# Optimization experiments

Measured on AMD Instinct MI355X. Metric: run time of the kernel, lower is better.

Reference implementation:

```python
import jax, jax.numpy as jnp
import numpy as np

B, NQ, NK, D = 4, 4096, 4096, 256


def setup_inputs() -> dict:
    key = jax.random.key(0)
    ks = jax.random.split(key, 14)
    s = 1.0 / np.sqrt(D)
    def lin(k):
        kw, kb = jax.random.split(k)
        return (jax.random.uniform(kw, (D, D), jnp.float32, -s, s),
                jax.random.uniform(kb, (D,), jnp.float32, -s, s))
    Wq, bq = lin(ks[0]); Wk, bk = lin(ks[1]); Wv, bv = lin(ks[2])
    W1, b1 = lin(ks[3]); W2, b2 = lin(ks[4]); W3, b3 = lin(ks[5])
    x = jax.random.normal(ks[6], (B, NK, D), jnp.float32)
    query = jax.random.normal(ks[7], (B, NQ, D), jnp.float32)
    return {"x": x, "query": query,
            "Wq": Wq, "bq": bq, "Wk": Wk, "bk": bk, "Wv": Wv, "bv": bv,
            "W1": W1, "b1": b1, "W2": W2, "b2": b2, "W3": W3, "b3": b3}


def reference(x, query, Wq, bq, Wk, bk, Wv, bv, W1, b1, W2, b2, W3, b3):
    # Linear: y = x @ W.T + b (torch convention)
    q = jnp.einsum('bnd,ed->bne', query, Wq) + bq   # [B,NQ,D]
    k = jnp.einsum('bnd,ed->bne', x, Wk) + bk       # [B,NK,D]
    v = jnp.einsum('bnd,ed->bne', x, Wv) + bv       # [B,NK,D]
    scale = 1.0 / jnp.sqrt(jnp.float32(x.shape[-1]))
    scores = jnp.einsum('bqd,bkd->bqk', q, k) * scale  # [B,NQ,NK]
    attn = jax.nn.softmax(scores, axis=-1)
    out = jnp.einsum('bqk,bkd->bqd', attn, v)          # [B,NQ,D]
    h = jax.nn.relu(jnp.einsum('bqd,ed->bqe', out, W1) + b1)
    h = jax.nn.relu(jnp.einsum('bqd,ed->bqe', h, W2) + b2)
    h = jax.nn.relu(jnp.einsum('bqd,ed->bqe', h, W3) + b3)
    return h, attn
```

## Files before the change

kernel.cpp:

```cpp
#include <hip/hip_runtime.h>

typedef _Float16 h16;
typedef __attribute__((ext_vector_type(4))) _Float16 h16x4;
typedef __attribute__((ext_vector_type(8))) _Float16 h16x8;
typedef __attribute__((ext_vector_type(4))) float f32x4;

#define NQD 4194304L
#define NROWS 16384L
#define NKK 4096L

static __device__ __forceinline__ f32x4 mfma16(h16x8 a, h16x8 b, f32x4 c) {
  return __builtin_amdgcn_mfma_f32_16x16x32_f16(a, b, c, 0, 0, 0);
}

__global__ void cast_weights(const float* __restrict__ w0, const float* __restrict__ w1,
                             const float* __restrict__ w2, const float* __restrict__ w3,
                             const float* __restrict__ w4, const float* __restrict__ w5,
                             h16* __restrict__ dst) {
  int wi = blockIdx.y;
  const float* src = wi == 0 ? w0 : wi == 1 ? w1 : wi == 2 ? w2 : wi == 3 ? w3 : wi == 4 ? w4 : w5;
  int c = blockIdx.x * 256 + threadIdx.x;
  float4 v = ((const float4*)src)[c];
  h16x4 h = {(h16)v.x, (h16)v.y, (h16)v.z, (h16)v.w};
  *(h16x4*)&dst[(long)wi * 65536 + (long)c * 4] = h;
}

__global__ __launch_bounds__(256) void qkv_proj(const float* __restrict__ x,
                                                const float* __restrict__ qry,
                                                const h16* __restrict__ wh,
                                                const float* __restrict__ bq,
                                                const float* __restrict__ bk,
                                                const float* __restrict__ bv,
                                                h16* __restrict__ qh,
                                                h16* __restrict__ kh,
                                                h16* __restrict__ vT) {
  const int z = blockIdx.z;
  const float* A = (z == 0) ? qry : x;
  const h16* W = wh + (long)z * 65536;
  const float* bias = (z == 0) ? bq : (z == 1) ? bk : bv;
  h16* outH = (z == 0) ? qh : (z == 1) ? kh : nullptr;
  h16* outT = (z == 2) ? vT : nullptr;

  __shared__ h16 As[128][72];
  __shared__ h16 Bs[64][72];
  const int tid = threadIdx.x;
  const int wave = tid >> 6, lane = tid & 63;
  const int quad = lane >> 4, l16 = lane & 15;
  const long arow0 = (long)blockIdx.x * 128;
  const int bn = blockIdx.y;
  f32x4 acc[2][4] = {};
  for (int k0 = 0; k0 < 256; k0 += 64) {
    #pragma unroll
    for (int it = 0; it < 8; ++it) {
      int c = it * 256 + tid;
      int r = c >> 4, c4 = (c & 15) * 4;
      float4 v = *(const float4*)&A[(arow0 + r) * 256 + k0 + c4];
      h16x4 h = {(h16)v.x, (h16)v.y, (h16)v.z, (h16)v.w};
      *(h16x4*)&As[r][c4] = h;
    }
    #pragma unroll
    for (int it = 0; it < 2; ++it) {
      int c = it * 256 + tid;
      int r = c >> 3, c8 = (c & 7) * 8;
      *(h16x8*)&Bs[r][c8] = *(const h16x8*)&W[(long)(bn * 64 + r) * 256 + k0 + c8];
    }
    __syncthreads();
    #pragma unroll
    for (int ks = 0; ks < 64; ks += 32) {
      h16x8 a[2], b[4];
      #pragma unroll
      for (int mi = 0; mi < 2; ++mi)
        a[mi] = *(const h16x8*)&As[wave * 32 + mi * 16 + l16][ks + quad * 8];
      #pragma unroll
      for (int ni = 0; ni < 4; ++ni)
        b[ni] = *(const h16x8*)&Bs[ni * 16 + l16][ks + quad * 8];
      #pragma unroll
      for (int mi = 0; mi < 2; ++mi)
        #pragma unroll
        for (int ni = 0; ni < 4; ++ni)
          acc[mi][ni] = mfma16(a[mi], b[ni], acc[mi][ni]);
    }
    __syncthreads();
  }
  #pragma unroll
  for (int mi = 0; mi < 2; ++mi) {
    #pragma unroll
    for (int ni = 0; ni < 4; ++ni) {
      int n = bn * 64 + ni * 16 + l16;
      float bv_ = bias[n];
      #pragma unroll
      for (int i = 0; i < 4; ++i) {
        long m = arow0 + wave * 32 + mi * 16 + quad * 4 + i;
        float v = acc[mi][ni][i] + bv_;
        if (outH) outH[m * 256 + n] = (h16)v;
        if (outT) outT[((m >> 12) * 256 + n) * 4096L + (m & 4095)] = (h16)v;
      }
    }
  }
}

__global__ __launch_bounds__(256) void gemm256(const h16* __restrict__ A,
                                               const h16* __restrict__ W,
                                               const float* __restrict__ bias,
                                               h16* __restrict__ outH,
                                               float* __restrict__ outF) {
  __shared__ h16 As[128][72];
  __shared__ h16 Bs[64][72];
  const int tid = threadIdx.x;
  const int wave = tid >> 6, lane = tid & 63;
  const int quad = lane >> 4, l16 = lane & 15;
  const long arow0 = (long)blockIdx.x * 128;
  const int bn = blockIdx.y;
  f32x4 acc[2][4] = {};
  for (int k0 = 0; k0 < 256; k0 += 64) {
    #pragma unroll
    for (int it = 0; it < 4; ++it) {
      int c = it * 256 + tid;
      int r = c >> 3, c8 = (c & 7) * 8;
      *(h16x8*)&As[r][c8] = *(const h16x8*)&A[(arow0 + r) * 256 + k0 + c8];
    }
    #pragma unroll
    for (int it = 0; it < 2; ++it) {
      int c = it * 256 + tid;
      int r = c >> 3, c8 = (c & 7) * 8;
      *(h16x8*)&Bs[r][c8] = *(const h16x8*)&W[(long)(bn * 64 + r) * 256 + k0 + c8];
    }
    __syncthreads();
    #pragma unroll
    for (int ks = 0; ks < 64; ks += 32) {
      h16x8 a[2], b[4];
      #pragma unroll
      for (int mi = 0; mi < 2; ++mi)
        a[mi] = *(const h16x8*)&As[wave * 32 + mi * 16 + l16][ks + quad * 8];
      #pragma unroll
      for (int ni = 0; ni < 4; ++ni)
        b[ni] = *(const h16x8*)&Bs[ni * 16 + l16][ks + quad * 8];
      #pragma unroll
      for (int mi = 0; mi < 2; ++mi)
        #pragma unroll
        for (int ni = 0; ni < 4; ++ni)
          acc[mi][ni] = mfma16(a[mi], b[ni], acc[mi][ni]);
    }
    __syncthreads();
  }
  #pragma unroll
  for (int mi = 0; mi < 2; ++mi) {
    #pragma unroll
    for (int ni = 0; ni < 4; ++ni) {
      int n = bn * 64 + ni * 16 + l16;
      float bv = bias[n];
      #pragma unroll
      for (int i = 0; i < 4; ++i) {
        long m = arow0 + wave * 32 + mi * 16 + quad * 4 + i;
        float v = fmaxf(acc[mi][ni][i] + bv, 0.0f);
        if (outH) outH[m * 256 + n] = (h16)v;
        if (outF) outF[m * 256 + n] = v;
      }
    }
  }
}

__global__ __launch_bounds__(256) void gemm_scores(const h16* __restrict__ qh,
                                                   const h16* __restrict__ kh,
                                                   float2* __restrict__ stats,
                                                   h16* __restrict__ Sh,
                                                   float* __restrict__ Sf) {
  __shared__ h16 As[128][72];
  __shared__ h16 Bs[128][72];
  const int tid = threadIdx.x;
  const int wave = tid >> 6, lane = tid & 63;
  const int quad = lane >> 4, l16 = lane & 15;
  const int bm = blockIdx.x, bn = blockIdx.y, b = blockIdx.z;
  const h16* Aq = qh + (long)b * 4096 * 256 + (long)bm * 128 * 256;
  const h16* Bk = kh + (long)b * 4096 * 256 + (long)bn * 128 * 256;
  f32x4 acc[2][8] = {};
  for (int k0 = 0; k0 < 256; k0 += 64) {
    #pragma unroll
    for (int it = 0; it < 4; ++it) {
      int c = it * 256 + tid;
      int r = c >> 3, c8 = (c & 7) * 8;
      *(h16x8*)&As[r][c8] = *(const h16x8*)&Aq[(long)r * 256 + k0 + c8];
      *(h16x8*)&Bs[r][c8] = *(const h16x8*)&Bk[(long)r * 256 + k0 + c8];
    }
    __syncthreads();
    #pragma unroll
    for (int ks = 0; ks < 64; ks += 32) {
      h16x8 a[2], bb[8];
      #pragma unroll
      for (int mi = 0; mi < 2; ++mi)
        a[mi] = *(const h16x8*)&As[wave * 32 + mi * 16 + l16][ks + quad * 8];
      #pragma unroll
      for (int ni = 0; ni < 8; ++ni)
        bb[ni] = *(const h16x8*)&Bs[ni * 16 + l16][ks + quad * 8];
      #pragma unroll
      for (int mi = 0; mi < 2; ++mi)
        #pragma unroll
        for (int ni = 0; ni < 8; ++ni)
          acc[mi][ni] = mfma16(a[mi], bb[ni], acc[mi][ni]);
    }
    __syncthreads();
  }
  #pragma unroll
  for (int mi = 0; mi < 2; ++mi)
    #pragma unroll
    for (int ni = 0; ni < 8; ++ni)
      #pragma unroll
      for (int i = 0; i < 4; ++i)
        acc[mi][ni][i] *= 0.0625f;
  #pragma unroll
  for (int mi = 0; mi < 2; ++mi) {
    #pragma unroll
    for (int i = 0; i < 4; ++i) {
      float mx = -1e30f;
      #pragma unroll
      for (int ni = 0; ni < 8; ++ni) mx = fmaxf(mx, acc[mi][ni][i]);
      #pragma unroll
      for (int off = 1; off < 16; off <<= 1) mx = fmaxf(mx, __shfl_xor(mx, off));
      float es = 0.0f;
      #pragma unroll
      for (int ni = 0; ni < 8; ++ni) es += __expf(acc[mi][ni][i] - mx);
      #pragma unroll
      for (int off = 1; off < 16; off <<= 1) es += __shfl_xor(es, off);
      if (l16 == 0) {
        long row = (long)b * 4096 + bm * 128 + wave * 32 + mi * 16 + quad * 4 + i;
        stats[row * 32 + bn] = make_float2(mx, es);
      }
    }
  }
  #pragma unroll
  for (int mi = 0; mi < 2; ++mi) {
    #pragma unroll
    for (int ni = 0; ni < 8; ++ni) {
      long col = (long)bn * 128 + ni * 16 + l16;
      #pragma unroll
      for (int i = 0; i < 4; ++i) {
        long row = (long)b * 4096 + bm * 128 + wave * 32 + mi * 16 + quad * 4 + i;
        if (Sh) Sh[row * 4096 + col] = (h16)acc[mi][ni][i];
        else    Sf[row * 4096 + col] = acc[mi][ni][i];
      }
    }
  }
}

__global__ __launch_bounds__(256) void rowstats_reduce(const float2* __restrict__ stats,
                                                       float2* __restrict__ rowstats) {
  const int tid = threadIdx.x;
  const int wave = tid >> 6, lane = tid & 63;
  const int j = lane & 31, rr = lane >> 5;
  const long base = (long)blockIdx.x * 256 + wave * 64;
  for (int it = 0; it < 32; ++it) {
    long row = base + it * 2 + rr;
    float2 s = stats[row * 32 + j];
    float m = s.x;
    #pragma unroll
    for (int off = 1; off < 32; off <<= 1) m = fmaxf(m, __shfl_xor(m, off));
    float e = s.y * __expf(s.x - m);
    #pragma unroll
    for (int off = 1; off < 32; off <<= 1) e += __shfl_xor(e, off);
    if (j == 0) rowstats[row] = make_float2(m, 1.0f / e);
  }
}

template <typename TS>
__global__ __launch_bounds__(256, 4) void gemm_av(const TS* __restrict__ S,
                                                  const h16* __restrict__ vT,
                                                  const float2* __restrict__ rowstats,
                                                  float* __restrict__ attn,
                                                  float* __restrict__ Opart,
                                                  h16* __restrict__ Odirect,
                                                  int KS) {
  __shared__ h16 As[64][40];
  __shared__ h16 Bs[256][40];
  const int tid = threadIdx.x;
  const int wave = tid >> 6, lane = tid & 63;
  const int quad = lane >> 4, l16 = lane & 15;
  const int mb = blockIdx.x, kc = blockIdx.y;
  const int KB = 4096 / KS;
  const long row0 = (long)mb * 64;
  const int b = mb >> 6;
  const h16* Vb = vT + (long)b * 256 * 4096;

  const int sr = tid >> 2, sc = (tid & 3) * 8;
  const long srow = row0 + sr;
  const float2 st = rowstats[srow];
  const TS* Srow = S + srow * 4096;
  float* Arow = attn + srow * 4096;

  f32x4 acc[4][4] = {};
  const int kbeg = kc * KB, kend = kbeg + KB;
  for (int k0 = kbeg; k0 < kend; k0 += 32) {
    float p[8];
    if constexpr (sizeof(TS) == 2) {
      h16x8 sv = *(const h16x8*)&Srow[k0 + sc];
      #pragma unroll
      for (int e = 0; e < 8; ++e) p[e] = __expf((float)sv[e] - st.x) * st.y;
    } else {
      float4 sa = *(const float4*)&Srow[k0 + sc];
      float4 sb = *(const float4*)&Srow[k0 + sc + 4];
      p[0] = __expf(sa.x - st.x) * st.y; p[1] = __expf(sa.y - st.x) * st.y;
      p[2] = __expf(sa.z - st.x) * st.y; p[3] = __expf(sa.w - st.x) * st.y;
      p[4] = __expf(sb.x - st.x) * st.y; p[5] = __expf(sb.y - st.x) * st.y;
      p[6] = __expf(sb.z - st.x) * st.y; p[7] = __expf(sb.w - st.x) * st.y;
    }
    float4 w0 = {p[0], p[1], p[2], p[3]}, w1 = {p[4], p[5], p[6], p[7]};
    *(float4*)&Arow[k0 + sc] = w0;
    *(float4*)&Arow[k0 + sc + 4] = w1;
    h16x8 ph = {(h16)p[0], (h16)p[1], (h16)p[2], (h16)p[3],
                (h16)p[4], (h16)p[5], (h16)p[6], (h16)p[7]};
    *(h16x8*)&As[sr][sc] = ph;
    #pragma unroll
    for (int it = 0; it < 4; ++it) {
      int d = it * 64 + (tid >> 2);
      *(h16x8*)&Bs[d][sc] = *(const h16x8*)&Vb[(long)d * 4096 + k0 + sc];
    }
    __syncthreads();
    h16x8 a[4], bb[4];
    #pragma unroll
    for (int mi = 0; mi < 4; ++mi)
      a[mi] = *(const h16x8*)&As[mi * 16 + l16][quad * 8];
    #pragma unroll
    for (int ni = 0; ni < 4; ++ni)
      bb[ni] = *(const h16x8*)&Bs[wave * 64 + ni * 16 + l16][quad * 8];
    #pragma unroll
    for (int mi = 0; mi < 4; ++mi)
      #pragma unroll
      for (int ni = 0; ni < 4; ++ni)
        acc[mi][ni] = mfma16(a[mi], bb[ni], acc[mi][ni]);
    __syncthreads();
  }
  #pragma unroll
  for (int mi = 0; mi < 4; ++mi) {
    #pragma unroll
    for (int ni = 0; ni < 4; ++ni) {
      int col = wave * 64 + ni * 16 + l16;
      #pragma unroll
      for (int i = 0; i < 4; ++i) {
        long row = row0 + mi * 16 + quad * 4 + i;
        if (Opart) Opart[((long)kc * NROWS + row) * 256 + col] = acc[mi][ni][i];
        else       Odirect[row * 256 + col] = (h16)acc[mi][ni][i];
      }
    }
  }
}

__global__ __launch_bounds__(256) void reduce_O(const float* __restrict__ Opart,
                                                h16* __restrict__ oh) {
  long i4 = (long)blockIdx.x * 256 + threadIdx.x;
  float4 s = {0, 0, 0, 0};
  #pragma unroll
  for (int kc = 0; kc < 4; ++kc) {
    float4 t = *(const float4*)&Opart[kc * NQD + i4 * 4];
    s.x += t.x; s.y += t.y; s.z += t.z; s.w += t.w;
  }
  h16x4 h = {(h16)s.x, (h16)s.y, (h16)s.z, (h16)s.w};
  *(h16x4*)&oh[i4 * 4] = h;
}

extern "C" void kernel_launch(void* const* d_in, const int* in_sizes, int n_in,
                              void* d_out, int out_size, void* d_ws, size_t ws_size,
                              hipStream_t stream) {
  (void)in_sizes; (void)n_in; (void)out_size;
  const float* x   = (const float*)d_in[0];
  const float* qry = (const float*)d_in[1];
  const float* Wq  = (const float*)d_in[2];  const float* bq = (const float*)d_in[3];
  const float* Wk  = (const float*)d_in[4];  const float* bk = (const float*)d_in[5];
  const float* Wv  = (const float*)d_in[6];  const float* bv = (const float*)d_in[7];
  const float* W1  = (const float*)d_in[8];  const float* b1 = (const float*)d_in[9];
  const float* W2  = (const float*)d_in[10]; const float* b2 = (const float*)d_in[11];
  const float* W3  = (const float*)d_in[12]; const float* b3 = (const float*)d_in[13];

  float* outH = (float*)d_out;
  float* attn = outH + NQD;

  char* w = (char*)d_ws;
  h16* qh = (h16*)w;
  h16* kh = qh + NQD;
  h16* vT = kh + NQD;
  h16* oh = vT + NQD;
  h16* h1 = oh + NQD;
  h16* h2 = h1 + NQD;
  h16* wh = h2 + NQD;
  size_t off_rs   = (size_t)(6 * NQD + 6 * 65536) * 2;
  size_t BASE     = off_rs + NROWS * 8;
  size_t statsB   = NROWS * 32 * 8;
  size_t ShB      = NROWS * NKK * 2;
  size_t OpartB   = 4 * NQD * 4;

  bool modeA = ws_size >= BASE + statsB + ShB + OpartB;
  bool modeB = !modeA && ws_size >= BASE + statsB + OpartB;

  float2* stats    = (modeA || modeB) ? (float2*)(w + BASE) : (float2*)oh;
  float2* rowstats = (modeA || modeB) ? (float2*)(w + off_rs) : (float2*)h2;
  h16*    Sh       = modeA ? (h16*)(w + BASE + statsB) : nullptr;
  float*  Opart    = modeA ? (float*)(w + BASE + statsB + ShB)
                   : modeB ? (float*)(w + BASE + statsB) : nullptr;
  int KS = (modeA || modeB) ? 4 : 1;

  cast_weights<<<dim3(64, 6), 256, 0, stream>>>(Wq, Wk, Wv, W1, W2, W3, wh);
  qkv_proj<<<dim3(128, 4, 3), 256, 0, stream>>>(x, qry, wh, bq, bk, bv, qh, kh, vT);
  gemm_scores<<<dim3(32, 32, 4), 256, 0, stream>>>(qh, kh, stats, Sh, modeA ? nullptr : attn);
  rowstats_reduce<<<dim3(64), 256, 0, stream>>>(stats, rowstats);
  if (modeA)
    gemm_av<h16><<<dim3(256, KS), 256, 0, stream>>>(Sh, vT, rowstats, attn, Opart, oh, KS);
  else
    gemm_av<float><<<dim3(256, KS), 256, 0, stream>>>(attn, vT, rowstats, attn, Opart, oh, KS);
  if (Opart)
    reduce_O<<<dim3(4096), 256, 0, stream>>>(Opart, oh);
  gemm256<<<dim3(128, 4), 256, 0, stream>>>(oh, wh + 3 * 65536, b1, h1, nullptr);
  gemm256<<<dim3(128, 4), 256, 0, stream>>>(h1, wh + 4 * 65536, b2, h2, nullptr);
  gemm256<<<dim3(128, 4), 256, 0, stream>>>(h2, wh + 5 * 65536, b3, nullptr, outH);
}
```

Baseline: 660.1 us.

## Fuse rowstats reduce into gemm_av, stage transposed/score stores through LDS, nontemporal attn writes

```diff
diff --git a/kernel.cpp b/kernel.cpp
--- a/kernel.cpp
+++ b/kernel.cpp
@@ -41,8 +41,9 @@
   h16* outH = (z == 0) ? qh : (z == 1) ? kh : nullptr;
   h16* outT = (z == 2) ? vT : nullptr;
 
-  __shared__ h16 As[128][72];
-  __shared__ h16 Bs[64][72];
+  __shared__ h16 smem[128 * 72 + 64 * 72];
+  h16 (*As)[72] = (h16(*)[72])smem;
+  h16 (*Bs)[72] = (h16(*)[72])(smem + 128 * 72);
   const int tid = threadIdx.x;
   const int wave = tid >> 6, lane = tid & 63;
   const int quad = lane >> 4, l16 = lane & 15;
@@ -82,19 +83,43 @@
     }
     __syncthreads();
   }
-  #pragma unroll
-  for (int mi = 0; mi < 2; ++mi) {
-    #pragma unroll
-    for (int ni = 0; ni < 4; ++ni) {
-      int n = bn * 64 + ni * 16 + l16;
-      float bv_ = bias[n];
-      #pragma unroll
-      for (int i = 0; i < 4; ++i) {
-        long m = arow0 + wave * 32 + mi * 16 + quad * 4 + i;
-        float v = acc[mi][ni][i] + bv_;
-        if (outH) outH[m * 256 + n] = (h16)v;
-        if (outT) outT[((m >> 12) * 256 + n) * 4096L + (m & 4095)] = (h16)v;
-      }
+  if (outH) {
+    #pragma unroll
+    for (int mi = 0; mi < 2; ++mi) {
+      #pragma unroll
+      for (int ni = 0; ni < 4; ++ni) {
+        int n = bn * 64 + ni * 16 + l16;
+        float bv_ = bias[n];
+        #pragma unroll
+        for (int i = 0; i < 4; ++i) {
+          long m = arow0 + wave * 32 + mi * 16 + quad * 4 + i;
+          outH[m * 256 + n] = (h16)(acc[mi][ni][i] + bv_);
+        }
+      }
+    }
+  } else {
+    h16* stg = smem;
+    #pragma unroll
+    for (int mi = 0; mi < 2; ++mi) {
+      #pragma unroll
+      for (int ni = 0; ni < 4; ++ni) {
+        int dl = ni * 16 + l16;
+        float bv_ = bias[bn * 64 + dl];
+        int mlb = wave * 32 + mi * 16 + quad * 4;
+        h16x4 hv = {(h16)(acc[mi][ni][0] + bv_), (h16)(acc[mi][ni][1] + bv_),
+                    (h16)(acc[mi][ni][2] + bv_), (h16)(acc[mi][ni][3] + bv_)};
+        *(h16x4*)&stg[dl * 136 + mlb] = hv;
+      }
+    }
+    __syncthreads();
+    const int bb = (int)(arow0 >> 12);
+    const long kb = arow0 & 4095;
+    #pragma unroll
+    for (int p = 0; p < 4; ++p) {
+      int d = p * 16 + (tid >> 4);
+      int c = (tid & 15) * 8;
+      h16x8 v = *(const h16x8*)&stg[d * 136 + c];
+      *(h16x8*)&outT[((long)bb * 256 + bn * 64 + d) * 4096 + kb + c] = v;
     }
   }
 }
@@ -165,8 +190,9 @@
                                                    float2* __restrict__ stats,
                                                    h16* __restrict__ Sh,
                                                    float* __restrict__ Sf) {
-  __shared__ h16 As[128][72];
-  __shared__ h16 Bs[128][72];
+  __shared__ h16 smem[128 * 72 * 2];
+  h16 (*As)[72] = (h16(*)[72])smem;
+  h16 (*Bs)[72] = (h16(*)[72])(smem + 128 * 72);
   const int tid = threadIdx.x;
   const int wave = tid >> 6, lane = tid & 63;
   const int quad = lane >> 4, l16 = lane & 15;
@@ -227,50 +253,57 @@
       }
     }
   }
-  #pragma unroll
-  for (int mi = 0; mi < 2; ++mi) {
-    #pragma unroll
-    for (int ni = 0; ni < 8; ++ni) {
-      long col = (long)bn * 128 + ni * 16 + l16;
-      #pragma unroll
-      for (int i = 0; i < 4; ++i) {
-        long row = (long)b * 4096 + bm * 128 + wave * 32 + mi * 16 + quad * 4 + i;
-        if (Sh) Sh[row * 4096 + col] = (h16)acc[mi][ni][i];
-        else    Sf[row * 4096 + col] = acc[mi][ni][i];
-      }
-    }
-  }
-}
-
-__global__ __launch_bounds__(256) void rowstats_reduce(const float2* __restrict__ stats,
-                                                       float2* __restrict__ rowstats) {
-  const int tid = threadIdx.x;
-  const int wave = tid >> 6, lane = tid & 63;
-  const int j = lane & 31, rr = lane >> 5;
-  const long base = (long)blockIdx.x * 256 + wave * 64;
-  for (int it = 0; it < 32; ++it) {
-    long row = base + it * 2 + rr;
-    float2 s = stats[row * 32 + j];
-    float m = s.x;
-    #pragma unroll
-    for (int off = 1; off < 32; off <<= 1) m = fmaxf(m, __shfl_xor(m, off));
-    float e = s.y * __expf(s.x - m);
-    #pragma unroll
-    for (int off = 1; off < 32; off <<= 1) e += __shfl_xor(e, off);
-    if (j == 0) rowstats[row] = make_float2(m, 1.0f / e);
+  if (Sh) {
+    h16* stg = smem;
+    #pragma unroll
+    for (int mi = 0; mi < 2; ++mi) {
+      #pragma unroll
+      for (int ni = 0; ni < 8; ++ni) {
+        int c = ni * 16 + l16;
+        #pragma unroll
+        for (int i = 0; i < 4; ++i) {
+          int r = wave * 32 + mi * 16 + quad * 4 + i;
+          stg[r * 136 + c] = (h16)acc[mi][ni][i];
+        }
+      }
+    }
+    __syncthreads();
+    const long rowbase = (long)b * 4096 + (long)bm * 128;
+    const long colbase = (long)bn * 128;
+    #pragma unroll
+    for (int p = 0; p < 8; ++p) {
+      int r = p * 16 + (tid >> 4);
+      int c = (tid & 15) * 8;
+      h16x8 v = *(const h16x8*)&stg[r * 136 + c];
+      *(h16x8*)&Sh[(rowbase + r) * 4096 + colbase + c] = v;
+    }
+  } else {
+    #pragma unroll
+    for (int mi = 0; mi < 2; ++mi) {
+      #pragma unroll
+      for (int ni = 0; ni < 8; ++ni) {
+        long col = (long)bn * 128 + ni * 16 + l16;
+        #pragma unroll
+        for (int i = 0; i < 4; ++i) {
+          long row = (long)b * 4096 + bm * 128 + wave * 32 + mi * 16 + quad * 4 + i;
+          Sf[row * 4096 + col] = acc[mi][ni][i];
+        }
+      }
+    }
   }
 }
 
 template <typename TS>
 __global__ __launch_bounds__(256, 4) void gemm_av(const TS* __restrict__ S,
                                                   const h16* __restrict__ vT,
-                                                  const float2* __restrict__ rowstats,
+                                                  const float2* __restrict__ stats,
                                                   float* __restrict__ attn,
                                                   float* __restrict__ Opart,
                                                   h16* __restrict__ Odirect,
                                                   int KS) {
   __shared__ h16 As[64][40];
   __shared__ h16 Bs[256][40];
+  __shared__ float2 rs[64];
   const int tid = threadIdx.x;
   const int wave = tid >> 6, lane = tid & 63;
   const int quad = lane >> 4, l16 = lane & 15;
@@ -280,9 +313,27 @@
   const int b = mb >> 6;
   const h16* Vb = vT + (long)b * 256 * 4096;
 
+  {
+    int r = tid >> 2, j = tid & 3;
+    const float2* sp = stats + (row0 + r) * 32 + j * 8;
+    float2 sv[8];
+    float m = -1e30f;
+    #pragma unroll
+    for (int t = 0; t < 8; ++t) { sv[t] = sp[t]; m = fmaxf(m, sv[t].x); }
+    m = fmaxf(m, __shfl_xor(m, 1));
+    m = fmaxf(m, __shfl_xor(m, 2));
+    float e = 0.0f;
+    #pragma unroll
+    for (int t = 0; t < 8; ++t) e += sv[t].y * __expf(sv[t].x - m);
+    e += __shfl_xor(e, 1);
+    e += __shfl_xor(e, 2);
+    if (j == 0) rs[r] = make_float2(m, 1.0f / e);
+  }
+  __syncthreads();
+
   const int sr = tid >> 2, sc = (tid & 3) * 8;
   const long srow = row0 + sr;
-  const float2 st = rowstats[srow];
+  const float2 st = rs[sr];
   const TS* Srow = S + srow * 4096;
   float* Arow = attn + srow * 4096;
 
@@ -302,9 +353,9 @@
       p[4] = __expf(sb.x - st.x) * st.y; p[5] = __expf(sb.y - st.x) * st.y;
       p[6] = __expf(sb.z - st.x) * st.y; p[7] = __expf(sb.w - st.x) * st.y;
     }
-    float4 w0 = {p[0], p[1], p[2], p[3]}, w1 = {p[4], p[5], p[6], p[7]};
-    *(float4*)&Arow[k0 + sc] = w0;
-    *(float4*)&Arow[k0 + sc + 4] = w1;
+    f32x4 w0 = {p[0], p[1], p[2], p[3]}, w1 = {p[4], p[5], p[6], p[7]};
+    __builtin_nontemporal_store(w0, (f32x4*)&Arow[k0 + sc]);
+    __builtin_nontemporal_store(w1, (f32x4*)&Arow[k0 + sc + 4]);
     h16x8 ph = {(h16)p[0], (h16)p[1], (h16)p[2], (h16)p[3],
                 (h16)p[4], (h16)p[5], (h16)p[6], (h16)p[7]};
     *(h16x8*)&As[sr][sc] = ph;
@@ -389,8 +440,7 @@
   bool modeA = ws_size >= BASE + statsB + ShB + OpartB;
   bool modeB = !modeA && ws_size >= BASE + statsB + OpartB;
 
-  float2* stats    = (modeA || modeB) ? (float2*)(w + BASE) : (float2*)oh;
-  float2* rowstats = (modeA || modeB) ? (float2*)(w + off_rs) : (float2*)h2;
+  float2* stats    = (modeA || modeB) ? (float2*)(w + BASE) : (float2*)h1;
   h16*    Sh       = modeA ? (h16*)(w + BASE + statsB) : nullptr;
   float*  Opart    = modeA ? (float*)(w + BASE + statsB + ShB)
                    : modeB ? (float*)(w + BASE + statsB) : nullptr;
@@ -399,11 +449,10 @@
   cast_weights<<<dim3(64, 6), 256, 0, stream>>>(Wq, Wk, Wv, W1, W2, W3, wh);
   qkv_proj<<<dim3(128, 4, 3), 256, 0, stream>>>(x, qry, wh, bq, bk, bv, qh, kh, vT);
   gemm_scores<<<dim3(32, 32, 4), 256, 0, stream>>>(qh, kh, stats, Sh, modeA ? nullptr : attn);
-  rowstats_reduce<<<dim3(64), 256, 0, stream>>>(stats, rowstats);
   if (modeA)
-    gemm_av<h16><<<dim3(256, KS), 256, 0, stream>>>(Sh, vT, rowstats, attn, Opart, oh, KS);
+    gemm_av<h16><<<dim3(256, KS), 256, 0, stream>>>(Sh, vT, stats, attn, Opart, oh, KS);
   else
-    gemm_av<float><<<dim3(256, KS), 256, 0, stream>>>(attn, vT, rowstats, attn, Opart, oh, KS);
+    gemm_av<float><<<dim3(256, KS), 256, 0, stream>>>(attn, vT, stats, attn, Opart, oh, KS);
   if (Opart)
     reduce_O<<<dim3(4096), 256, 0, stream>>>(Opart, oh);
   gemm256<<<dim3(128, 4), 256, 0, stream>>>(oh, wh + 3 * 65536, b1, h1, nullptr);
```

Result: faster. 583.6 us (-11.6%).
